# Kernel tuning notes

Measured on AMD Instinct MI355X. Metric: run time of the kernel, lower is better.

Reference implementation:

```python
import jax, jax.numpy as jnp
import numpy as np

D_MODEL = 768
NUM_HEADS = 12
D_K = D_MODEL // NUM_HEADS


def setup_inputs() -> dict:
    key = jax.random.key(0)
    ks = jax.random.split(key, 9)
    B, S = 2, 4096
    x = jax.random.normal(ks[0], (B, S, D_MODEL), dtype=jnp.float32)
    s = 1.0 / np.sqrt(D_MODEL)
    Wq = jax.random.normal(ks[1], (D_MODEL, D_MODEL), dtype=jnp.float32) * s
    Wk = jax.random.normal(ks[2], (D_MODEL, D_MODEL), dtype=jnp.float32) * s
    Wv = jax.random.normal(ks[3], (D_MODEL, D_MODEL), dtype=jnp.float32) * s
    Wo = jax.random.normal(ks[4], (D_MODEL, D_MODEL), dtype=jnp.float32) * s
    bq = jnp.zeros((D_MODEL,), dtype=jnp.float32)
    bk = jnp.zeros((D_MODEL,), dtype=jnp.float32)
    bv = jnp.zeros((D_MODEL,), dtype=jnp.float32)
    bo = jnp.zeros((D_MODEL,), dtype=jnp.float32)
    return {"x": x, "Wq": Wq, "bq": bq, "Wk": Wk, "bk": bk,
            "Wv": Wv, "bv": bv, "Wo": Wo, "bo": bo}


def _split_heads(t):
    B, S, _ = t.shape
    return t.reshape(B, S, NUM_HEADS, D_K).transpose(0, 2, 1, 3)  # [B,H,S,d_k]


def reference(x, Wq, bq, Wk, bk, Wv, bv, Wo, bo):
    Q = _split_heads(x @ Wq.T + bq)
    K = _split_heads(x @ Wk.T + bk)
    V = _split_heads(x @ Wv.T + bv)
    scale = 1.0 / jnp.sqrt(jnp.float32(D_K))
    scores = jnp.einsum('bhqd,bhkd->bhqk', Q, K) * scale  # [B,H,S,S]
    attn = jax.nn.softmax(scores, axis=-1)
    out = jnp.einsum('bhqk,bhkd->bhqd', attn, V)          # [B,H,S,d_k]
    B, _, S, _ = out.shape
    out = out.transpose(0, 2, 1, 3).reshape(B, S, D_MODEL)
    return out @ Wo.T + bo
```

## Files before the change

kernel.cpp:

```cpp
#include <hip/hip_runtime.h>
#include <hip/hip_bf16.h>
#include <stdint.h>

typedef __hip_bfloat16 bf16;
typedef __attribute__((ext_vector_type(8))) short short8;
typedef __attribute__((ext_vector_type(4))) float f32x4;
typedef __attribute__((ext_vector_type(16))) float f32x16;

#define MFMA16(a, b, c) __builtin_amdgcn_mfma_f32_16x16x32_bf16((a), (b), (c), 0, 0, 0)
#define MFMA32(a, b, c) __builtin_amdgcn_mfma_f32_32x32x16_bf16((a), (b), (c), 0, 0, 0)

__device__ __forceinline__ unsigned short f2bf(float f) {
  bf16 h = __float2bfloat16(f);
  unsigned short u;
  __builtin_memcpy(&u, &h, 2);
  return u;
}

__device__ __forceinline__ uint32_t cvtpk(float lo, float hi) {
  uint32_t r;
  asm("v_cvt_pk_bf16_f32 %0, %1, %2" : "=v"(r) : "v"(lo), "v"(hi));
  return r;
}

__device__ __forceinline__ void pl32swap(uint32_t& a, uint32_t& b) {
  asm volatile("v_permlane32_swap_b32 %0, %1" : "+v"(a), "+v"(b));
}

__device__ __forceinline__ void gload_lds16(const void* g, void* l) {
  __builtin_amdgcn_global_load_lds(
      (const __attribute__((address_space(1))) uint32_t*)g,
      (__attribute__((address_space(3))) uint32_t*)l, 16, 0, 0);
}

__device__ __forceinline__ int swz_chunk(int row, int c) { return c ^ (row & 7); }

__global__ __launch_bounds__(256) void cvt_kernel(const float* __restrict__ in,
                                                  bf16* __restrict__ out, int n4) {
  int i = blockIdx.x * blockDim.x + threadIdx.x;
  int stride = gridDim.x * blockDim.x;
  for (; i < n4; i += stride) {
    float4 v = ((const float4*)in)[i];
    ushort4 u;
    u.x = f2bf(v.x); u.y = f2bf(v.y); u.z = f2bf(v.z); u.w = f2bf(v.w);
    ((ushort4*)out)[i] = u;
  }
}

__global__ __launch_bounds__(256) void cvtw_kernel(
    const float* __restrict__ w0, const float* __restrict__ w1,
    const float* __restrict__ w2, const float* __restrict__ w3,
    bf16* __restrict__ o0, bf16* __restrict__ o1,
    bf16* __restrict__ o2, bf16* __restrict__ o3) {
  int idx = blockIdx.x * 256 + threadIdx.x;
  int w = idx / 147456, i = idx - w * 147456;
  const float* src = (w == 0) ? w0 : (w == 1) ? w1 : (w == 2) ? w2 : w3;
  bf16* dst = (w == 0) ? o0 : (w == 1) ? o1 : (w == 2) ? o2 : o3;
  float4 v = ((const float4*)src)[i];
  ushort4 u;
  u.x = f2bf(v.x); u.y = f2bf(v.y); u.z = f2bf(v.z); u.w = f2bf(v.w);
  ((ushort4*)dst)[i] = u;
}

__global__ __launch_bounds__(256) void gemm_qkv(
    const bf16* __restrict__ A,
    const bf16* __restrict__ Wqb, const bf16* __restrict__ Wkb,
    const bf16* __restrict__ Wvb,
    const float* __restrict__ bq, const float* __restrict__ bk,
    const float* __restrict__ bv,
    bf16* __restrict__ Qh, bf16* __restrict__ Kh, bf16* __restrict__ Vh,
    float sq) {
  __shared__ bf16 As[128 * 32];
  __shared__ bf16 Bs[128 * 32];
  const int tid = threadIdx.x;
  const int lane = tid & 63, wid = tid >> 6;
  const int wr = wid >> 1, wc = wid & 1;
  const int l15 = lane & 15, lhi = lane >> 4;
  const int tm = blockIdx.x * 128;
  const int by = blockIdx.y;
  const int seg = by / 6;
  const int tn = (by - seg * 6) * 128;

  const bf16* B = (seg == 0) ? Wqb : (seg == 1) ? Wkb : Wvb;
  const float* bias = (seg == 0) ? bq : (seg == 1) ? bk : bv;
  bf16* dst = (seg == 0) ? Qh : (seg == 1) ? Kh : Vh;
  const float scale = (seg == 0) ? sq : 1.0f;
  const int K = 768;

  f32x4 zero = {0.f, 0.f, 0.f, 0.f};
  f32x4 acc[4][4];
  for (int i = 0; i < 4; ++i)
    for (int j = 0; j < 4; ++j) acc[i][j] = zero;

  for (int k0 = 0; k0 < K; k0 += 32) {
    __syncthreads();
    for (int it = 0; it < 2; ++it) {
      int o = (tid + it * 256) << 4;
      int row = o >> 6, cb = o & 63;
      gload_lds16((const char*)A + (((size_t)(tm + row) * K + k0) << 1) + cb, (char*)As + o);
      gload_lds16((const char*)B + (((size_t)(tn + row) * K + k0) << 1) + cb, (char*)Bs + o);
    }
    __syncthreads();
    short8 af[4], bfr[4];
    for (int mi = 0; mi < 4; ++mi)
      af[mi] = *(const short8*)((const char*)As + ((wr * 64 + mi * 16 + l15) << 6) + (lhi << 4));
    for (int ni = 0; ni < 4; ++ni)
      bfr[ni] = *(const short8*)((const char*)Bs + ((wc * 64 + ni * 16 + l15) << 6) + (lhi << 4));
    for (int mi = 0; mi < 4; ++mi)
      for (int ni = 0; ni < 4; ++ni)
        acc[mi][ni] = MFMA16(af[mi], bfr[ni], acc[mi][ni]);
  }

  for (int mi = 0; mi < 4; ++mi)
    for (int ni = 0; ni < 4; ++ni)
      for (int j = 0; j < 4; ++j) {
        int m = tm + wr * 64 + mi * 16 + lhi * 4 + j;
        int n = tn + wc * 64 + ni * 16 + l15;
        float v = (acc[mi][ni][j] + bias[n]) * scale;
        int b = m >> 12, s = m & 4095, h = n >> 6, d = n & 63;
        dst[(((size_t)(b * 12 + h) * 4096 + s) << 6) + d] = __float2bfloat16(v);
      }
}

__global__ __launch_bounds__(256) void gemm_wo(
    const bf16* __restrict__ A, const bf16* __restrict__ B,
    const float* __restrict__ bias, float* __restrict__ C) {
  __shared__ bf16 As[128 * 32];
  __shared__ bf16 Bs[64 * 32];
  const int tid = threadIdx.x;
  const int lane = tid & 63, wid = tid >> 6;
  const int l15 = lane & 15, lhi = lane >> 4;
  const int tm = blockIdx.x * 128, tn = blockIdx.y * 64;
  const int K = 768;

  f32x4 zero = {0.f, 0.f, 0.f, 0.f};
  f32x4 acc[2][4];
  for (int i = 0; i < 2; ++i)
    for (int j = 0; j < 4; ++j) acc[i][j] = zero;

  for (int k0 = 0; k0 < K; k0 += 32) {
    __syncthreads();
    for (int it = 0; it < 2; ++it) {
      int o = (tid + it * 256) << 4;
      int row = o >> 6, cb = o & 63;
      gload_lds16((const char*)A + (((size_t)(tm + row) * K + k0) << 1) + cb, (char*)As + o);
    }
    {
      int o = tid << 4;
      int row = o >> 6, cb = o & 63;
      gload_lds16((const char*)B + (((size_t)(tn + row) * K + k0) << 1) + cb, (char*)Bs + o);
    }
    __syncthreads();
    short8 af[2], bfr[4];
    for (int mi = 0; mi < 2; ++mi)
      af[mi] = *(const short8*)((const char*)As + ((wid * 32 + mi * 16 + l15) << 6) + (lhi << 4));
    for (int ni = 0; ni < 4; ++ni)
      bfr[ni] = *(const short8*)((const char*)Bs + ((ni * 16 + l15) << 6) + (lhi << 4));
    for (int mi = 0; mi < 2; ++mi)
      for (int ni = 0; ni < 4; ++ni)
        acc[mi][ni] = MFMA16(af[mi], bfr[ni], acc[mi][ni]);
  }

  for (int mi = 0; mi < 2; ++mi)
    for (int ni = 0; ni < 4; ++ni)
      for (int j = 0; j < 4; ++j) {
        int m = tm + wid * 32 + mi * 16 + lhi * 4 + j;
        int n = tn + ni * 16 + l15;
        C[(size_t)m * 768 + n] = acc[mi][ni][j] + bias[n];
      }
}

__global__ __launch_bounds__(256) void transpose_v(const bf16* __restrict__ Vh,
                                                   bf16* __restrict__ VTh) {
  __shared__ bf16 T[64 * 64];
  const int tid = threadIdx.x;
  const int bh = blockIdx.x >> 6;
  const int t = blockIdx.x & 63;
  const char* src = (const char*)(Vh + ((size_t)bh * 4096 + t * 64) * 64);
  char* dst = (char*)(VTh + ((size_t)bh * 64) * 4096 + t * 64);

  for (int it = 0; it < 2; ++it) {
    int idx = tid + it * 256;
    int r = idx & 63, cc = idx >> 6;
    uint4 vv = *(const uint4*)(src + r * 128 + cc * 16);
    unsigned short sv[8];
    __builtin_memcpy(sv, &vv, 16);
#pragma unroll
    for (int jj = 0; jj < 8; ++jj) {
      int d = cc * 8 + jj;
      *(unsigned short*)((char*)T + d * 128 + (swz_chunk(d, r >> 3) << 4) +
                         ((r & 7) << 1)) = sv[jj];
    }
  }
  __syncthreads();
  for (int it = 0; it < 2; ++it) {
    int idx = tid + it * 256;
    int d = idx >> 3, c = idx & 7;
    uint4 vv = *(const uint4*)((const char*)T + d * 128 + (swz_chunk(d, c) << 4));
    *(uint4*)(dst + (size_t)d * 8192 + c * 16) = vv;
  }
}

__global__ __launch_bounds__(256, 3) void attn_kernel(
    const bf16* __restrict__ Qh, const bf16* __restrict__ Kh,
    const bf16* __restrict__ VTh, bf16* __restrict__ AO) {
  __shared__ float4 smem4[34816 / 16];
  char* smraw = (char*)smem4;
#define KT(b) (smraw + (b) * 8192)
#define VT(b) (smraw + 16384 + (b) * 8192)
  float* OX = (float*)smraw;

  const int tid = threadIdx.x;
  const int lane = tid & 63, wid = tid >> 6;
  const int l31 = lane & 31, h = lane >> 5;
  const int qsub = wid & 1, kvh = wid >> 1;

  const int bh = blockIdx.x >> 5;
  const int qt = blockIdx.x & 31;

  const size_t hb = (size_t)bh * 4096 * 64;
  const bf16* Qb = Qh + hb;
  const bf16* Kb = Kh + hb;
  const char* Vg0 = (const char*)(VTh + hb);
  const int qb = qt * 128 + qsub * 64;

  short8 qf[2][4];
#pragma unroll
  for (int j = 0; j < 2; ++j)
#pragma unroll
    for (int ki = 0; ki < 4; ++ki)
      qf[j][ki] = *(const short8*)((const char*)Qb + (size_t)(qb + 32 * j + l31) * 128 +
                                   ki * 32 + h * 16);

  f32x16 z16;
  for (int i = 0; i < 16; ++i) z16[i] = 0.f;
  f32x16 o00 = z16, o01 = z16, o10 = z16, o11 = z16;
  float psum0 = 0.f, psum1 = 0.f;

  const int krow = kvh * 32 + l31;

  for (int it = 0; it < 2; ++it) {
    int o = (tid + it * 256) << 4;
    int row = o >> 7, c = (o >> 4) & 7;
    int sw = swz_chunk(row, c) << 4;
    gload_lds16((const char*)Kb + row * 128 + sw, KT(0) + o);
    gload_lds16(Vg0 + row * 8192 + sw, VT(0) + o);
  }
  __syncthreads();

  int cur = 0;
  for (int kt = 0; kt < 64; ++kt) {
    if (kt < 63) {
      const char* Kg = (const char*)(Kb + (size_t)(kt + 1) * 4096);
      const char* Vg = Vg0 + (size_t)(kt + 1) * 128;
      char* Kd = KT(cur ^ 1);
      char* Vd = VT(cur ^ 1);
      for (int it = 0; it < 2; ++it) {
        int o = (tid + it * 256) << 4;
        int row = o >> 7, c = (o >> 4) & 7;
        int sw = swz_chunk(row, c) << 4;
        gload_lds16(Kg + row * 128 + sw, Kd + o);
        gload_lds16(Vg + row * 8192 + sw, Vd + o);
      }
    }

    const char* Kl = KT(cur);
    const char* Vl = VT(cur);

    f32x16 s0, s1;
    {
      short8 kf = *(const short8*)(Kl + krow * 128 + (swz_chunk(krow, h) << 4));
      s0 = MFMA32(kf, qf[0][0], z16);
      s1 = MFMA32(kf, qf[1][0], z16);
    }
#pragma unroll
    for (int ki = 1; ki < 4; ++ki) {
      short8 kf = *(const short8*)(Kl + krow * 128 + (swz_chunk(krow, 2 * ki + h) << 4));
      s0 = MFMA32(kf, qf[0][ki], s0);
      s1 = MFMA32(kf, qf[1][ki], s1);
    }

    short8 pb[2][2];
#pragma unroll
    for (int j = 0; j < 2; ++j) {
#pragma unroll
      for (int kk = 0; kk < 2; ++kk) {
        float p[8];
#pragma unroll
        for (int e = 0; e < 8; ++e)
          p[e] = __builtin_amdgcn_exp2f(j ? s1[8 * kk + e] : s0[8 * kk + e]);
        float ps = ((p[0] + p[1]) + (p[2] + p[3])) + ((p[4] + p[5]) + (p[6] + p[7]));
        if (j) psum1 += ps; else psum0 += ps;
        uint32_t A0 = cvtpk(p[0], p[1]), A1 = cvtpk(p[2], p[3]);
        uint32_t B0 = cvtpk(p[4], p[5]), B1 = cvtpk(p[6], p[7]);
        pl32swap(A0, B0);
        pl32swap(A1, B1);
        uint32_t w[4] = {A0, A1, B0, B1};
        short8 frag;
        __builtin_memcpy(&frag, w, 16);
        pb[j][kk] = frag;
      }
    }

#pragma unroll
    for (int kk = 0; kk < 2; ++kk) {
      short8 v0 = *(const short8*)(Vl + l31 * 128 +
                                   (swz_chunk(l31, 4 * kvh + 2 * kk + h) << 4));
      short8 v1 = *(const short8*)(Vl + (32 + l31) * 128 +
                                   (swz_chunk(32 + l31, 4 * kvh + 2 * kk + h) << 4));
      o00 = MFMA32(v0, pb[0][kk], o00);
      o01 = MFMA32(v0, pb[1][kk], o01);
      o10 = MFMA32(v1, pb[0][kk], o10);
      o11 = MFMA32(v1, pb[1][kk], o11);
    }

    __syncthreads();
    cur ^= 1;
  }

  psum0 += __shfl_xor(psum0, 32);
  psum1 += __shfl_xor(psum1, 32);

  float* W = OX + (size_t)(qsub * 64 + lane) * 68;
  if (kvh == 1) {
#pragma unroll
    for (int g = 0; g < 4; ++g) {
      *(float4*)(W + 0 * 16 + 4 * g) = make_float4(o00[4*g], o00[4*g+1], o00[4*g+2], o00[4*g+3]);
      *(float4*)(W + 1 * 16 + 4 * g) = make_float4(o01[4*g], o01[4*g+1], o01[4*g+2], o01[4*g+3]);
      *(float4*)(W + 2 * 16 + 4 * g) = make_float4(o10[4*g], o10[4*g+1], o10[4*g+2], o10[4*g+3]);
      *(float4*)(W + 3 * 16 + 4 * g) = make_float4(o11[4*g], o11[4*g+1], o11[4*g+2], o11[4*g+3]);
    }
    W[64] = psum0;
    W[65] = psum1;
  }
  __syncthreads();
  if (kvh == 0) {
#pragma unroll
    for (int g = 0; g < 4; ++g) {
      float4 a0 = *(const float4*)(W + 0 * 16 + 4 * g);
      float4 a1 = *(const float4*)(W + 1 * 16 + 4 * g);
      float4 a2 = *(const float4*)(W + 2 * 16 + 4 * g);
      float4 a3 = *(const float4*)(W + 3 * 16 + 4 * g);
      o00[4*g] += a0.x; o00[4*g+1] += a0.y; o00[4*g+2] += a0.z; o00[4*g+3] += a0.w;
      o01[4*g] += a1.x; o01[4*g+1] += a1.y; o01[4*g+2] += a1.z; o01[4*g+3] += a1.w;
      o10[4*g] += a2.x; o10[4*g+1] += a2.y; o10[4*g+2] += a2.z; o10[4*g+3] += a2.w;
      o11[4*g] += a3.x; o11[4*g+1] += a3.y; o11[4*g+2] += a3.z; o11[4*g+3] += a3.w;
    }
    psum0 += W[64];
    psum1 += W[65];
    float pinv0 = 1.0f / psum0;
    float pinv1 = 1.0f / psum1;

    const int b = bh / 12, hd = bh % 12;
#pragma unroll
    for (int j = 0; j < 2; ++j) {
      int q = qb + 32 * j + l31;
      char* base = (char*)AO + (((size_t)(b * 4096 + q)) * 768 + hd * 64) * 2;
      float pv = j ? pinv1 : pinv0;
#pragma unroll
      for (int t = 0; t < 2; ++t) {
#pragma unroll
        for (int u = 0; u < 4; ++u) {
          ushort4 us;
          float v0 = (t ? (j ? o11[4*u+0] : o10[4*u+0]) : (j ? o01[4*u+0] : o00[4*u+0]));
          float v1 = (t ? (j ? o11[4*u+1] : o10[4*u+1]) : (j ? o01[4*u+1] : o00[4*u+1]));
          float v2 = (t ? (j ? o11[4*u+2] : o10[4*u+2]) : (j ? o01[4*u+2] : o00[4*u+2]));
          float v3 = (t ? (j ? o11[4*u+3] : o10[4*u+3]) : (j ? o01[4*u+3] : o00[4*u+3]));
          us.x = f2bf(v0 * pv);
          us.y = f2bf(v1 * pv);
          us.z = f2bf(v2 * pv);
          us.w = f2bf(v3 * pv);
          int d0 = 32 * t + 8 * u + 4 * h;
          *(ushort4*)(base + d0 * 2) = us;
        }
      }
    }
  }
#undef KT
#undef VT
}

extern "C" void kernel_launch(void* const* d_in, const int* in_sizes, int n_in,
                              void* d_out, int out_size, void* d_ws, size_t ws_size,
                              hipStream_t stream) {
  (void)in_sizes; (void)n_in; (void)out_size; (void)ws_size;
  const float* x  = (const float*)d_in[0];
  const float* Wq = (const float*)d_in[1];
  const float* bq = (const float*)d_in[2];
  const float* Wk = (const float*)d_in[3];
  const float* bk = (const float*)d_in[4];
  const float* Wv = (const float*)d_in[5];
  const float* bv = (const float*)d_in[6];
  const float* Wo = (const float*)d_in[7];
  const float* bo = (const float*)d_in[8];

  char* ws = (char*)d_ws;
  bf16* Qh  = (bf16*)(ws + 0);
  bf16* Kh  = (bf16*)(ws + 12582912);
  bf16* Vh  = (bf16*)(ws + 25165824);
  bf16* xb  = (bf16*)(ws + 37748736);
  bf16* Wqb = (bf16*)(ws + 50331648);
  bf16* Wkb = (bf16*)(ws + 51511296);
  bf16* Wvb = (bf16*)(ws + 52690944);
  bf16* Wob = (bf16*)(ws + 53870592);
  bf16* VTh = xb;
  bf16* AO  = Vh;

  cvt_kernel<<<6144, 256, 0, stream>>>(x, xb, 1572864);
  cvtw_kernel<<<2304, 256, 0, stream>>>(Wq, Wk, Wv, Wo, Wqb, Wkb, Wvb, Wob);

  const float SQ = 0.125f * 1.4426950408889634f;
  dim3 gq(64, 18);
  gemm_qkv<<<gq, 256, 0, stream>>>(xb, Wqb, Wkb, Wvb, bq, bk, bv,
                                   Qh, Kh, Vh, SQ);
  transpose_v<<<1536, 256, 0, stream>>>(Vh, VTh);
  attn_kernel<<<768, 256, 0, stream>>>(Qh, Kh, VTh, AO);
  dim3 gw(64, 12);
  gemm_wo<<<gw, 256, 0, stream>>>(AO, Wob, bo, (float*)d_out);
}
```

Baseline: 208.2 us.

## Merge conversion kernels, deepen GEMM K-tiles with swizzle, add MFMA priority hints

```diff
diff --git a/kernel.cpp b/kernel.cpp
--- a/kernel.cpp
+++ b/kernel.cpp
@@ -35,34 +35,33 @@
 
 __device__ __forceinline__ int swz_chunk(int row, int c) { return c ^ (row & 7); }
 
-__global__ __launch_bounds__(256) void cvt_kernel(const float* __restrict__ in,
-                                                  bf16* __restrict__ out, int n4) {
-  int i = blockIdx.x * blockDim.x + threadIdx.x;
-  int stride = gridDim.x * blockDim.x;
-  for (; i < n4; i += stride) {
-    float4 v = ((const float4*)in)[i];
-    ushort4 u;
-    u.x = f2bf(v.x); u.y = f2bf(v.y); u.z = f2bf(v.z); u.w = f2bf(v.w);
-    ((ushort4*)out)[i] = u;
-  }
-}
-
-__global__ __launch_bounds__(256) void cvtw_kernel(
+__global__ __launch_bounds__(256) void cvt_all(
+    const float* __restrict__ x,
     const float* __restrict__ w0, const float* __restrict__ w1,
     const float* __restrict__ w2, const float* __restrict__ w3,
+    bf16* __restrict__ xo,
     bf16* __restrict__ o0, bf16* __restrict__ o1,
     bf16* __restrict__ o2, bf16* __restrict__ o3) {
   int idx = blockIdx.x * 256 + threadIdx.x;
-  int w = idx / 147456, i = idx - w * 147456;
-  const float* src = (w == 0) ? w0 : (w == 1) ? w1 : (w == 2) ? w2 : w3;
-  bf16* dst = (w == 0) ? o0 : (w == 1) ? o1 : (w == 2) ? o2 : o3;
+  const float* src;
+  bf16* dst;
+  int i;
+  if (idx < 1572864) {
+    src = x; dst = xo; i = idx;
+  } else {
+    int r = idx - 1572864;
+    int w = r / 147456;
+    i = r - w * 147456;
+    src = (w == 0) ? w0 : (w == 1) ? w1 : (w == 2) ? w2 : w3;
+    dst = (w == 0) ? o0 : (w == 1) ? o1 : (w == 2) ? o2 : o3;
+  }
   float4 v = ((const float4*)src)[i];
   ushort4 u;
   u.x = f2bf(v.x); u.y = f2bf(v.y); u.z = f2bf(v.z); u.w = f2bf(v.w);
   ((ushort4*)dst)[i] = u;
 }
 
-__global__ __launch_bounds__(256) void gemm_qkv(
+__global__ __launch_bounds__(256, 4) void gemm_qkv(
     const bf16* __restrict__ A,
     const bf16* __restrict__ Wqb, const bf16* __restrict__ Wkb,
     const bf16* __restrict__ Wvb,
@@ -70,8 +69,8 @@
     const float* __restrict__ bv,
     bf16* __restrict__ Qh, bf16* __restrict__ Kh, bf16* __restrict__ Vh,
     float sq) {
-  __shared__ bf16 As[128 * 32];
-  __shared__ bf16 Bs[128 * 32];
+  __shared__ bf16 As[128 * 64];
+  __shared__ bf16 Bs[128 * 64];
   const int tid = threadIdx.x;
   const int lane = tid & 63, wid = tid >> 6;
   const int wr = wid >> 1, wc = wid & 1;
@@ -92,23 +91,32 @@
   for (int i = 0; i < 4; ++i)
     for (int j = 0; j < 4; ++j) acc[i][j] = zero;
 
-  for (int k0 = 0; k0 < K; k0 += 32) {
+  for (int k0 = 0; k0 < K; k0 += 64) {
     __syncthreads();
-    for (int it = 0; it < 2; ++it) {
+    for (int it = 0; it < 4; ++it) {
       int o = (tid + it * 256) << 4;
-      int row = o >> 6, cb = o & 63;
-      gload_lds16((const char*)A + (((size_t)(tm + row) * K + k0) << 1) + cb, (char*)As + o);
-      gload_lds16((const char*)B + (((size_t)(tn + row) * K + k0) << 1) + cb, (char*)Bs + o);
+      int row = o >> 7, c = (o >> 4) & 7;
+      int sw = swz_chunk(row, c) << 4;
+      gload_lds16((const char*)A + (((size_t)(tm + row) * K + k0) << 1) + sw, (char*)As + o);
+      gload_lds16((const char*)B + (((size_t)(tn + row) * K + k0) << 1) + sw, (char*)Bs + o);
     }
     __syncthreads();
-    short8 af[4], bfr[4];
-    for (int mi = 0; mi < 4; ++mi)
-      af[mi] = *(const short8*)((const char*)As + ((wr * 64 + mi * 16 + l15) << 6) + (lhi << 4));
-    for (int ni = 0; ni < 4; ++ni)
-      bfr[ni] = *(const short8*)((const char*)Bs + ((wc * 64 + ni * 16 + l15) << 6) + (lhi << 4));
-    for (int mi = 0; mi < 4; ++mi)
-      for (int ni = 0; ni < 4; ++ni)
-        acc[mi][ni] = MFMA16(af[mi], bfr[ni], acc[mi][ni]);
+    for (int ks = 0; ks < 2; ++ks) {
+      short8 af[4], bfr[4];
+      for (int mi = 0; mi < 4; ++mi) {
+        int row = wr * 64 + mi * 16 + l15;
+        af[mi] = *(const short8*)((const char*)As + row * 128 +
+                                  (swz_chunk(row, ks * 4 + lhi) << 4));
+      }
+      for (int ni = 0; ni < 4; ++ni) {
+        int row = wc * 64 + ni * 16 + l15;
+        bfr[ni] = *(const short8*)((const char*)Bs + row * 128 +
+                                   (swz_chunk(row, ks * 4 + lhi) << 4));
+      }
+      for (int mi = 0; mi < 4; ++mi)
+        for (int ni = 0; ni < 4; ++ni)
+          acc[mi][ni] = MFMA16(af[mi], bfr[ni], acc[mi][ni]);
+    }
   }
 
   for (int mi = 0; mi < 4; ++mi)
@@ -122,11 +130,11 @@
       }
 }
 
-__global__ __launch_bounds__(256) void gemm_wo(
+__global__ __launch_bounds__(256, 4) void gemm_wo(
     const bf16* __restrict__ A, const bf16* __restrict__ B,
     const float* __restrict__ bias, float* __restrict__ C) {
-  __shared__ bf16 As[128 * 32];
-  __shared__ bf16 Bs[64 * 32];
+  __shared__ bf16 As[128 * 64];
+  __shared__ bf16 Bs[64 * 64];
   const int tid = threadIdx.x;
   const int lane = tid & 63, wid = tid >> 6;
   const int l15 = lane & 15, lhi = lane >> 4;
@@ -138,27 +146,37 @@
   for (int i = 0; i < 2; ++i)
     for (int j = 0; j < 4; ++j) acc[i][j] = zero;
 
-  for (int k0 = 0; k0 < K; k0 += 32) {
+  for (int k0 = 0; k0 < K; k0 += 64) {
     __syncthreads();
+    for (int it = 0; it < 4; ++it) {
+      int o = (tid + it * 256) << 4;
+      int row = o >> 7, c = (o >> 4) & 7;
+      int sw = swz_chunk(row, c) << 4;
+      gload_lds16((const char*)A + (((size_t)(tm + row) * K + k0) << 1) + sw, (char*)As + o);
+    }
     for (int it = 0; it < 2; ++it) {
       int o = (tid + it * 256) << 4;
-      int row = o >> 6, cb = o & 63;
-      gload_lds16((const char*)A + (((size_t)(tm + row) * K + k0) << 1) + cb, (char*)As + o);
-    }
-    {
-      int o = tid << 4;
-      int row = o >> 6, cb = o & 63;
-      gload_lds16((const char*)B + (((size_t)(tn + row) * K + k0) << 1) + cb, (char*)Bs + o);
+      int row = o >> 7, c = (o >> 4) & 7;
+      int sw = swz_chunk(row, c) << 4;
+      gload_lds16((const char*)B + (((size_t)(tn + row) * K + k0) << 1) + sw, (char*)Bs + o);
     }
     __syncthreads();
-    short8 af[2], bfr[4];
-    for (int mi = 0; mi < 2; ++mi)
-      af[mi] = *(const short8*)((const char*)As + ((wid * 32 + mi * 16 + l15) << 6) + (lhi << 4));
-    for (int ni = 0; ni < 4; ++ni)
-      bfr[ni] = *(const short8*)((const char*)Bs + ((ni * 16 + l15) << 6) + (lhi << 4));
-    for (int mi = 0; mi < 2; ++mi)
-      for (int ni = 0; ni < 4; ++ni)
-        acc[mi][ni] = MFMA16(af[mi], bfr[ni], acc[mi][ni]);
+    for (int ks = 0; ks < 2; ++ks) {
+      short8 af[2], bfr[4];
+      for (int mi = 0; mi < 2; ++mi) {
+        int row = wid * 32 + mi * 16 + l15;
+        af[mi] = *(const short8*)((const char*)As + row * 128 +
+                                  (swz_chunk(row, ks * 4 + lhi) << 4));
+      }
+      for (int ni = 0; ni < 4; ++ni) {
+        int row = ni * 16 + l15;
+        bfr[ni] = *(const short8*)((const char*)Bs + row * 128 +
+                                   (swz_chunk(row, ks * 4 + lhi) << 4));
+      }
+      for (int mi = 0; mi < 2; ++mi)
+        for (int ni = 0; ni < 4; ++ni)
+          acc[mi][ni] = MFMA16(af[mi], bfr[ni], acc[mi][ni]);
+    }
   }
 
   for (int mi = 0; mi < 2; ++mi)
@@ -268,6 +286,7 @@
     const char* Vl = VT(cur);
 
     f32x16 s0, s1;
+    __builtin_amdgcn_s_setprio(1);
     {
       short8 kf = *(const short8*)(Kl + krow * 128 + (swz_chunk(krow, h) << 4));
       s0 = MFMA32(kf, qf[0][0], z16);
@@ -279,6 +298,7 @@
       s0 = MFMA32(kf, qf[0][ki], s0);
       s1 = MFMA32(kf, qf[1][ki], s1);
     }
+    __builtin_amdgcn_s_setprio(0);
 
     short8 pb[2][2];
 #pragma unroll
@@ -302,6 +322,7 @@
       }
     }
 
+    __builtin_amdgcn_s_setprio(1);
 #pragma unroll
     for (int kk = 0; kk < 2; ++kk) {
       short8 v0 = *(const short8*)(Vl + l31 * 128 +
@@ -313,6 +334,7 @@
       o10 = MFMA32(v1, pb[0][kk], o10);
       o11 = MFMA32(v1, pb[1][kk], o11);
     }
+    __builtin_amdgcn_s_setprio(0);
 
     __syncthreads();
     cur ^= 1;
@@ -406,8 +428,7 @@
   bf16* VTh = xb;
   bf16* AO  = Vh;
 
-  cvt_kernel<<<6144, 256, 0, stream>>>(x, xb, 1572864);
-  cvtw_kernel<<<2304, 256, 0, stream>>>(Wq, Wk, Wv, Wo, Wqb, Wkb, Wvb, Wob);
+  cvt_all<<<8448, 256, 0, stream>>>(x, Wq, Wk, Wv, Wo, xb, Wqb, Wkb, Wvb, Wob);
 
   const float SQ = 0.125f * 1.4426950408889634f;
   dim3 gq(64, 18);
```

Result: faster. 189.0 us (-9.2%).
